# Kernel optimization log

Measured on AMD Instinct MI355X. Metric: run time of the kernel, lower is better.

Reference implementation:

```python
import jax, jax.numpy as jnp
import numpy as np

N, E, G, L, D = 50000, 800000, 512, 3, 128
BN_EPS = 1e-5


def setup_inputs() -> dict:
    key = jax.random.key(0)
    ks = jax.random.split(key, 16)
    x = jax.random.normal(ks[0], (N, D), dtype=jnp.float32)
    edge_index = jax.random.randint(ks[1], (2, E), 0, N)
    batch = jnp.sort(jax.random.randint(ks[2], (N,), 0, G))
    W1 = jax.random.normal(ks[3], (L, D, D), dtype=jnp.float32) * 0.05
    b1 = jax.random.normal(ks[4], (L, D), dtype=jnp.float32) * 0.05
    gamma = jax.random.uniform(ks[5], (L, D), dtype=jnp.float32) + 0.5
    beta = jax.random.normal(ks[6], (L, D), dtype=jnp.float32) * 0.05
    running_mean = jax.random.normal(ks[7], (L, D), dtype=jnp.float32) * 0.1
    running_var = jax.random.uniform(ks[8], (L, D), dtype=jnp.float32) + 0.5
    W2 = jax.random.normal(ks[9], (L, D, D), dtype=jnp.float32) * 0.05
    b2 = jax.random.normal(ks[10], (L, D), dtype=jnp.float32) * 0.05
    lin1_W = jax.random.normal(ks[11], (L * D, L * D), dtype=jnp.float32) * 0.05
    lin1_b = jax.random.normal(ks[12], (L * D,), dtype=jnp.float32) * 0.05
    lin2_W = jax.random.normal(ks[13], (L * D, 10), dtype=jnp.float32) * 0.05
    lin2_b = jax.random.normal(ks[14], (10,), dtype=jnp.float32) * 0.05
    return {"x": x, "edge_index": edge_index, "batch": batch,
            "W1": W1, "b1": b1, "gamma": gamma, "beta": beta,
            "running_mean": running_mean, "running_var": running_var,
            "W2": W2, "b2": b2, "lin1_W": lin1_W, "lin1_b": lin1_b,
            "lin2_W": lin2_W, "lin2_b": lin2_b}


def _gin_layer(h, src, dst, W1, b1, gamma, beta, rm, rv, W2, b2):
    # GINConv (eps=0): MLP((1+eps)*x + sum_{j->i} x_j); aggregate src->dst
    agg = jax.ops.segment_sum(h[src], dst, num_segments=N)  # [N, D]
    z = (h + agg) @ W1 + b1
    # BatchNorm1d in eval mode (running stats)
    z = (z - rm) * (gamma / jnp.sqrt(rv + BN_EPS)) + beta
    z = jax.nn.relu(z)
    return jax.nn.relu(z @ W2 + b2)


def reference(x, edge_index, batch, W1, b1, gamma, beta, running_mean,
              running_var, W2, b2, lin1_W, lin1_b, lin2_W, lin2_b):
    src, dst = edge_index[0], edge_index[1]
    h = x
    pooled = []
    for i in range(L):
        h = _gin_layer(h, src, dst, W1[i], b1[i], gamma[i], beta[i],
                       running_mean[i], running_var[i], W2[i], b2[i])
        pooled.append(jax.ops.segment_sum(h, batch, num_segments=G))  # [G, D]
    g = jnp.concatenate(pooled, axis=1)  # [G, L*D]
    g = jax.nn.relu(g @ lin1_W + lin1_b)
    # dropout is identity in eval mode
    return g @ lin2_W + lin2_b  # [G, num_classes]
```

## Files before the change

### kernel.cpp

```cpp
#include <hip/hip_runtime.h>
#include <hip/hip_bf16.h>

#define D_FEAT 128
#define N_GRAPHS 512
#define N_LAYERS 3
#define POOL_DIM (N_LAYERS * D_FEAT)
#define N_CLASSES 10
#define BN_EPS 1e-5f
#define CAP 64
#define NBINS 8
#define SLABCAP 768


typedef __attribute__((ext_vector_type(8))) short bf16x8;
typedef __attribute__((ext_vector_type(8))) unsigned short ushort8;
typedef __attribute__((ext_vector_type(4))) float f32x4;

__device__ __forceinline__ unsigned short f2bf(float f) {
    unsigned u = __builtin_bit_cast(unsigned, f);
    u += 0x7FFFu + ((u >> 16) & 1u);
    return (unsigned short)(u >> 16);
}
__device__ __forceinline__ float bf2f(unsigned short h) {
    unsigned u = ((unsigned)h) << 16;
    return __builtin_bit_cast(float, u);
}
__device__ __forceinline__ float bf_lo(unsigned u) {
    return __builtin_bit_cast(float, u << 16);
}
__device__ __forceinline__ float bf_hi(unsigned u) {
    return __builtin_bit_cast(float, u & 0xffff0000u);
}

__global__ __launch_bounds__(256) void setup_kernel(
        const float* __restrict__ x, unsigned short* __restrict__ xb,
        const float* __restrict__ W1, const float* __restrict__ W2,
        unsigned short* __restrict__ Wt,
        const float* __restrict__ b1, const float* __restrict__ gamma,
        const float* __restrict__ beta, const float* __restrict__ rm,
        const float* __restrict__ rv, const float* __restrict__ b2,
        float* __restrict__ ea, float* __restrict__ eb,
        int* __restrict__ cursor, float* __restrict__ pooled,
        const int* __restrict__ ei, int2* __restrict__ pairs,
        int* __restrict__ cnts, int E,
        int N, int n4, int B0, int B1, int B2, int B3, int B4) {
    int b = blockIdx.x, tid = threadIdx.x;
    if (b < B0) {
        int i = b * 256 + tid;
        if (i < n4) {
            float4 v = ((const float4*)x)[i];
            ushort4 o;
            o.x = f2bf(v.x); o.y = f2bf(v.y); o.z = f2bf(v.z); o.w = f2bf(v.w);
            ((ushort4*)xb)[i] = o;
        }
    } else if (b < B1) {
        __shared__ float tile[64][65];
        int t = b - B0;
        int slot = t >> 2;
        int r0 = ((t >> 1) & 1) * 64;
        int c0 = (t & 1) * 64;
        int l = slot >> 1;
        const float* W = (slot & 1) ? W2 : W1;
        const float* Wb = W + (size_t)l * D_FEAT * D_FEAT;
        int rr = tid >> 2, cc4 = (tid & 3) * 16;
        #pragma unroll
        for (int j = 0; j < 16; ++j)
            tile[rr][cc4 + j] = Wb[(size_t)(r0 + rr) * D_FEAT + c0 + cc4 + j];
        __syncthreads();
        int nn = tid >> 2, kk4 = (tid & 3) * 16;
        unsigned short* Wo = Wt + (size_t)slot * D_FEAT * D_FEAT;
        #pragma unroll
        for (int j = 0; j < 16; ++j)
            Wo[(size_t)(c0 + nn) * D_FEAT + r0 + kk4 + j] = f2bf(tile[kk4 + j][nn]);
    } else if (b < B2) {
        int i = (b - B1) * 256 + tid;
        if (i < N_LAYERS * D_FEAT) {
            int l = i >> 7, c = i & 127;
            float s = gamma[i] * rsqrtf(rv[i] + BN_EPS);
            ea[(2 * l) * D_FEAT + c] = s;
            eb[(2 * l) * D_FEAT + c] = (b1[i] - rm[i]) * s + beta[i];
            ea[(2 * l + 1) * D_FEAT + c] = 1.0f;
            eb[(2 * l + 1) * D_FEAT + c] = b2[i];
        }
    } else if (b < B3) {
        int i = (b - B2) * 256 + tid;
        if (i < N) cursor[i] = 0;
    } else if (b < B4) {
        int i = (b - B3) * 256 + tid;
        if (i < N_GRAPHS * POOL_DIM) pooled[i] = 0.f;
    } else {
        __shared__ int loc[NBINS];
        int bb = b - B4;
        int per = (E + 255) / 256;
        int e0 = bb * per;
        int e1 = e0 + per; if (e1 > E) e1 = E;
        int span = (N + NBINS - 1) / NBINS;
        if (tid < NBINS) loc[tid] = 0;
        __syncthreads();
        for (int e = e0 + tid; e < e1; e += 256) {
            int dst = ei[E + e];
            int src = ei[e];
            int bin = dst / span;
            int p = atomicAdd(&loc[bin], 1);
            if (p < SLABCAP)
                pairs[((size_t)(bin * 256 + bb)) * SLABCAP + p] = make_int2(src, dst);
        }
        __syncthreads();
        if (tid < NBINS)
            cnts[tid * 256 + bb] = loc[tid];
    }
}

__global__ __launch_bounds__(256) void fill_v3(const int2* __restrict__ pairs,
                                               const int* __restrict__ cnts,
                                               int* __restrict__ cursor,
                                               int* __restrict__ bucket) {
    int r = blockIdx.x & 7;
    int chunk = blockIdx.x >> 3;
    #pragma unroll
    for (int s = 0; s < 4; ++s) {
        int blk = chunk * 4 + s;
        int cnt = cnts[r * 256 + blk];
        if (cnt > SLABCAP) cnt = SLABCAP;
        const int2* slab = pairs + (size_t)(r * 256 + blk) * SLABCAP;
        for (int p = threadIdx.x; p < cnt; p += 256) {
            int2 pr = slab[p];
            int pos = atomicAdd(&cursor[pr.y], 1);
            if (pos < CAP) bucket[(size_t)pr.y * CAP + pos] = pr.x;
        }
    }
}

__global__ __launch_bounds__(256) void agg_kernel(const unsigned short* __restrict__ hprev,
                                                  const int* __restrict__ deg,
                                                  const int* __restrict__ bucket,
                                                  unsigned short* __restrict__ y, int n) {
    int wave = threadIdx.x >> 6, lane = threadIdx.x & 63;
    int n0 = (blockIdx.x * 4 + wave) * 2;
    if (n0 >= n) return;
    int n1 = n0 + 1;
    bool v1 = (n1 < n);
    int d0 = deg[n0]; if (d0 > CAP) d0 = CAP;
    int d1 = v1 ? deg[n1] : 0; if (d1 > CAP) d1 = CAP;
    int grp = lane >> 4, sub = lane & 15;
    const uint4* hp = (const uint4*)hprev;

    int idx0 = bucket[(size_t)n0 * CAP + lane];
    int idx1 = v1 ? bucket[(size_t)n1 * CAP + lane] : 0;

    uint4 s0v = hp[(size_t)n0 * 16 + sub];
    uint4 s1v = v1 ? hp[(size_t)n1 * 16 + sub] : make_uint4(0u, 0u, 0u, 0u);

    float a0[8] = {0.f,0.f,0.f,0.f,0.f,0.f,0.f,0.f};
    float a1[8] = {0.f,0.f,0.f,0.f,0.f,0.f,0.f,0.f};
    int dmax = d0 > d1 ? d0 : d1;

    auto issue = [&](int t, bool (&p0)[4], bool (&p1)[4],
                     uint4 (&w0)[4], uint4 (&w1)[4]) {
        #pragma unroll
        for (int q = 0; q < 4; ++q) {
            int e = t + q * 4 + grp;
            int s0 = __shfl(idx0, e & 63);
            int s1 = __shfl(idx1, e & 63);
            p0[q] = e < d0;
            p1[q] = e < d1;
            int r0 = p0[q] ? s0 : n0;
            int r1 = p1[q] ? s1 : n0;
            w0[q] = hp[(size_t)r0 * 16 + sub];
            w1[q] = hp[(size_t)r1 * 16 + sub];
        }
    };
    auto accum = [&](bool (&p0)[4], bool (&p1)[4],
                     uint4 (&w0)[4], uint4 (&w1)[4]) {
        #pragma unroll
        for (int q = 0; q < 4; ++q) {
            if (p0[q]) {
                uint4 v = w0[q];
                a0[0] += bf_lo(v.x); a0[1] += bf_hi(v.x);
                a0[2] += bf_lo(v.y); a0[3] += bf_hi(v.y);
                a0[4] += bf_lo(v.z); a0[5] += bf_hi(v.z);
                a0[6] += bf_lo(v.w); a0[7] += bf_hi(v.w);
            }
            if (p1[q]) {
                uint4 v = w1[q];
                a1[0] += bf_lo(v.x); a1[1] += bf_hi(v.x);
                a1[2] += bf_lo(v.y); a1[3] += bf_hi(v.y);
                a1[4] += bf_lo(v.z); a1[5] += bf_hi(v.z);
                a1[6] += bf_lo(v.w); a1[7] += bf_hi(v.w);
            }
        }
    };

    if (dmax > 0) {
        bool cp0[4], cp1[4];
        uint4 cw0[4], cw1[4];
        issue(0, cp0, cp1, cw0, cw1);
        for (int t = 16; t < dmax; t += 16) {
            bool np0[4], np1[4];
            uint4 nw0[4], nw1[4];
            issue(t, np0, np1, nw0, nw1);
            accum(cp0, cp1, cw0, cw1);
            #pragma unroll
            for (int q = 0; q < 4; ++q) {
                cp0[q] = np0[q]; cp1[q] = np1[q];
                cw0[q] = nw0[q]; cw1[q] = nw1[q];
            }
        }
        accum(cp0, cp1, cw0, cw1);
    }

    #pragma unroll
    for (int j = 0; j < 8; ++j) {
        a0[j] += __shfl_xor(a0[j], 16);
        a0[j] += __shfl_xor(a0[j], 32);
        a1[j] += __shfl_xor(a1[j], 16);
        a1[j] += __shfl_xor(a1[j], 32);
    }

    a0[0] += bf_lo(s0v.x); a0[1] += bf_hi(s0v.x);
    a0[2] += bf_lo(s0v.y); a0[3] += bf_hi(s0v.y);
    a0[4] += bf_lo(s0v.z); a0[5] += bf_hi(s0v.z);
    a0[6] += bf_lo(s0v.w); a0[7] += bf_hi(s0v.w);
    if (v1) {
        a1[0] += bf_lo(s1v.x); a1[1] += bf_hi(s1v.x);
        a1[2] += bf_lo(s1v.y); a1[3] += bf_hi(s1v.y);
        a1[4] += bf_lo(s1v.z); a1[5] += bf_hi(s1v.z);
        a1[6] += bf_lo(s1v.w); a1[7] += bf_hi(s1v.w);
    }

    if (grp == 0) {
        uint4 o;
        o.x = (unsigned)f2bf(a0[0]) | ((unsigned)f2bf(a0[1]) << 16);
        o.y = (unsigned)f2bf(a0[2]) | ((unsigned)f2bf(a0[3]) << 16);
        o.z = (unsigned)f2bf(a0[4]) | ((unsigned)f2bf(a0[5]) << 16);
        o.w = (unsigned)f2bf(a0[6]) | ((unsigned)f2bf(a0[7]) << 16);
        ((uint4*)y)[(size_t)n0 * 16 + sub] = o;
        if (v1) {
            uint4 p;
            p.x = (unsigned)f2bf(a1[0]) | ((unsigned)f2bf(a1[1]) << 16);
            p.y = (unsigned)f2bf(a1[2]) | ((unsigned)f2bf(a1[3]) << 16);
            p.z = (unsigned)f2bf(a1[4]) | ((unsigned)f2bf(a1[5]) << 16);
            p.w = (unsigned)f2bf(a1[6]) | ((unsigned)f2bf(a1[7]) << 16);
            ((uint4*)y)[(size_t)n1 * 16 + sub] = p;
        }
    }
}

__global__ __launch_bounds__(256) void layer_fused(const unsigned short* __restrict__ A,
                                                   const unsigned short* __restrict__ Wt1,
                                                   const unsigned short* __restrict__ Wt2,
                                                   const float* __restrict__ ea1,
                                                   const float* __restrict__ eb1,
                                                   const float* __restrict__ ea2,
                                                   const float* __restrict__ eb2,
                                                   const int* __restrict__ batch,
                                                   float* __restrict__ pooled, int loff,
                                                   unsigned short* __restrict__ outh, int n) {
    __shared__ unsigned short As[64][136];
    __shared__ unsigned short Ws[128][136];
    int tid = threadIdx.x;
    int row0 = blockIdx.x * 64;
    int wave = tid >> 6, lane = tid & 63;
    int m0 = wave * 16;
    int lrow = lane & 15, lq = lane >> 4;

    #pragma unroll
    for (int i = 0; i < 4; ++i) {
        int idx = tid + i * 256;
        int r = idx >> 4, c = (idx & 15) * 8;
        ushort8 v = (ushort8)0;
        if (row0 + r < n) v = *(const ushort8*)&A[(size_t)(row0 + r) * D_FEAT + c];
        *(ushort8*)&As[r][c] = v;
    }
    #pragma unroll
    for (int i = 0; i < 8; ++i) {
        int idx = tid + i * 256;
        int r = idx >> 4, c = (idx & 15) * 8;
        *(ushort8*)&Ws[r][c] = *(const ushort8*)&Wt1[(size_t)r * D_FEAT + c];
    }

    ushort8 w2reg[8];
    #pragma unroll
    for (int i = 0; i < 8; ++i) {
        int idx = tid + i * 256;
        int r = idx >> 4, c = (idx & 15) * 8;
        w2reg[i] = *(const ushort8*)&Wt2[(size_t)r * D_FEAT + c];
    }

    int gr0 = row0 + m0 + lq * 4;
    int bq[4];
    if (gr0 + 3 < n) {
        int4 b4 = *(const int4*)&batch[gr0];
        bq[0] = b4.x; bq[1] = b4.y; bq[2] = b4.z; bq[3] = b4.w;
    } else {
        #pragma unroll
        for (int r = 0; r < 4; ++r)
            bq[r] = (gr0 + r < n) ? batch[gr0 + r] : -1;
    }
    __syncthreads();

    f32x4 acc[8] = {};
    #pragma unroll
    for (int t = 0; t < 4; ++t) {
        bf16x8 a = *(const bf16x8*)&As[m0 + lrow][t * 32 + lq * 8];
        #pragma unroll
        for (int nt = 0; nt < 8; ++nt) {
            bf16x8 b = *(const bf16x8*)&Ws[nt * 16 + lrow][t * 32 + lq * 8];
            acc[nt] = __builtin_amdgcn_mfma_f32_16x16x32_bf16(a, b, acc[nt], 0, 0, 0);
        }
    }
    __syncthreads();

    #pragma unroll
    for (int nt = 0; nt < 8; ++nt) {
        int col = nt * 16 + lrow;
        float al = ea1[col], be = eb1[col];
        #pragma unroll
        for (int r = 0; r < 4; ++r) {
            float v = fmaxf(fmaf(acc[nt][r], al, be), 0.f);
            As[m0 + lq * 4 + r][col] = f2bf(v);
        }
    }
    #pragma unroll
    for (int i = 0; i < 8; ++i) {
        int idx = tid + i * 256;
        int r = idx >> 4, c = (idx & 15) * 8;
        *(ushort8*)&Ws[r][c] = w2reg[i];
    }
    __syncthreads();

    f32x4 acc2[8] = {};
    #pragma unroll
    for (int t = 0; t < 4; ++t) {
        bf16x8 a = *(const bf16x8*)&As[m0 + lrow][t * 32 + lq * 8];
        #pragma unroll
        for (int nt = 0; nt < 8; ++nt) {
            bf16x8 b = *(const bf16x8*)&Ws[nt * 16 + lrow][t * 32 + lq * 8];
            acc2[nt] = __builtin_amdgcn_mfma_f32_16x16x32_bf16(a, b, acc2[nt], 0, 0, 0);
        }
    }

    float vv[8][4];
    #pragma unroll
    for (int nt = 0; nt < 8; ++nt) {
        int col = nt * 16 + lrow;
        float al = ea2[col], be = eb2[col];
        #pragma unroll
        for (int r = 0; r < 4; ++r) {
            unsigned short hb = f2bf(fmaxf(fmaf(acc2[nt][r], al, be), 0.f));
            vv[nt][r] = bf2f(hb);
            if (outh) {
                int grow = row0 + m0 + lq * 4 + r;
                if (grow < n) outh[(size_t)grow * D_FEAT + col] = hb;
            }
        }
    }

    int gmn = 0x7fffffff, gmx = -1;
    #pragma unroll
    for (int r = 0; r < 4; ++r) {
        if (bq[r] >= 0) {
            gmn = bq[r] < gmn ? bq[r] : gmn;
            gmx = bq[r] > gmx ? bq[r] : gmx;
        }
    }
    {
        int t;
        t = __shfl_xor(gmn, 16); gmn = t < gmn ? t : gmn;
        t = __shfl_xor(gmn, 32); gmn = t < gmn ? t : gmn;
        t = __shfl_xor(gmx, 16); gmx = t > gmx ? t : gmx;
        t = __shfl_xor(gmx, 32); gmx = t > gmx ? t : gmx;
    }
    for (int seg = gmn; seg <= gmx; ++seg) {
        #pragma unroll
        for (int nt = 0; nt < 8; ++nt) {
            float s = 0.f;
            #pragma unroll
            for (int r = 0; r < 4; ++r)
                if (bq[r] == seg) s += vv[nt][r];
            s += __shfl_xor(s, 16);
            s += __shfl_xor(s, 32);
            if (lq == 0 && s != 0.f)
                atomicAdd(&pooled[(size_t)seg * POOL_DIM + loff + nt * 16 + lrow], s);
        }
    }
}

__global__ __launch_bounds__(384) void head_kernel(const float* __restrict__ pooled,
                                                   const float* __restrict__ W1,
                                                   const float* __restrict__ b1v,
                                                   const float* __restrict__ W2,
                                                   const float* __restrict__ b2v,
                                                   float* __restrict__ out) {
    __shared__ float f1[4][POOL_DIM];
    int j = threadIdx.x;
    int g0 = blockIdx.x * 4;
    const float* pr = pooled + (size_t)g0 * POOL_DIM;
    float bb = b1v[j];
    float s0 = bb, s1 = bb, s2 = bb, s3 = bb;
    for (int k0 = 0; k0 < POOL_DIM; k0 += 8) {
        float w[8];
        #pragma unroll
        for (int i = 0; i < 8; ++i)
            w[i] = W1[(size_t)(k0 + i) * POOL_DIM + j];
        #pragma unroll
        for (int i = 0; i < 8; ++i) {
            int k = k0 + i;
            s0 = fmaf(pr[k],                w[i], s0);
            s1 = fmaf(pr[POOL_DIM + k],     w[i], s1);
            s2 = fmaf(pr[2 * POOL_DIM + k], w[i], s2);
            s3 = fmaf(pr[3 * POOL_DIM + k], w[i], s3);
        }
    }
    f1[0][j] = fmaxf(s0, 0.f);
    f1[1][j] = fmaxf(s1, 0.f);
    f1[2][j] = fmaxf(s2, 0.f);
    f1[3][j] = fmaxf(s3, 0.f);
    __syncthreads();
    if (j < 4 * N_CLASSES) {
        int g = j / N_CLASSES, c = j % N_CLASSES;
        float s = b2v[c];
        for (int k = 0; k < POOL_DIM; ++k)
            s = fmaf(f1[g][k], W2[(size_t)k * N_CLASSES + c], s);
        out[(size_t)(g0 + g) * N_CLASSES + c] = s;
    }
}

extern "C" void kernel_launch(void* const* d_in, const int* in_sizes, int n_in,
                              void* d_out, int out_size, void* d_ws, size_t ws_size,
                              hipStream_t stream) {
    const float* x      = (const float*)d_in[0];
    const int*   ei     = (const int*)  d_in[1];
    const int*   batch  = (const int*)  d_in[2];
    const float* W1     = (const float*)d_in[3];
    const float* b1     = (const float*)d_in[4];
    const float* gamma  = (const float*)d_in[5];
    const float* beta   = (const float*)d_in[6];
    const float* rm     = (const float*)d_in[7];
    const float* rv     = (const float*)d_in[8];
    const float* W2     = (const float*)d_in[9];
    const float* b2     = (const float*)d_in[10];
    const float* lin1W  = (const float*)d_in[11];
    const float* lin1b  = (const float*)d_in[12];
    const float* lin2W  = (const float*)d_in[13];
    const float* lin2b  = (const float*)d_in[14];
    float* out = (float*)d_out;

    const int N = in_sizes[0] / D_FEAT;
    const int E = in_sizes[1] / 2;

    char* ws = (char*)d_ws;
    auto carve = [&](size_t bytes) {
        char* p = ws;
        ws += (bytes + 255) & ~(size_t)255;
        return p;
    };
    int*   cursor    = (int*)  carve((size_t)N * 4);
    int*   cnts      = (int*)  carve((size_t)NBINS * 256 * 4);
    int*   bucket    = (int*)  carve((size_t)N * CAP * 4);
    int2*  pairs     = (int2*) carve((size_t)NBINS * 256 * SLABCAP * 8);
    float* ea        = (float*)carve((size_t)2 * N_LAYERS * D_FEAT * 4);
    float* eb        = (float*)carve((size_t)2 * N_LAYERS * D_FEAT * 4);
    unsigned short* Wt   = (unsigned short*)carve((size_t)2 * N_LAYERS * D_FEAT * D_FEAT * 2);
    unsigned short* xb   = (unsigned short*)carve((size_t)N * D_FEAT * 2);
    unsigned short* ybuf = (unsigned short*)carve((size_t)N * D_FEAT * 2);
    unsigned short* hbuf = (unsigned short*)carve((size_t)N * D_FEAT * 2);
    float* pooled    = (float*)carve((size_t)N_GRAPHS * POOL_DIM * 4);

    const int n4 = N * D_FEAT / 4;
    const int B0 = (n4 + 255) / 256;
    const int B1 = B0 + 24;
    const int B2 = B1 + 2;
    const int B3 = B2 + (N + 255) / 256;
    const int B4 = B3 + (N_GRAPHS * POOL_DIM + 255) / 256;
    const int B5 = B4 + 256;

    setup_kernel<<<B5, 256, 0, stream>>>(x, xb, W1, W2, Wt, b1, gamma, beta,
                                         rm, rv, b2, ea, eb, cursor, pooled,
                                         ei, pairs, cnts, E,
                                         N, n4, B0, B1, B2, B3, B4);
    fill_v3<<<8 * 64, 256, 0, stream>>>(pairs, cnts, cursor, bucket);

    const unsigned short* hprev = xb;
    for (int l = 0; l < N_LAYERS; ++l) {
        agg_kernel<<<(N + 7) / 8, 256, 0, stream>>>(hprev, cursor, bucket, ybuf, N);
        unsigned short* outh = (l == N_LAYERS - 1) ? nullptr : hbuf;
        layer_fused<<<(N + 63) / 64, 256, 0, stream>>>(ybuf,
                      Wt + (size_t)(2 * l) * D_FEAT * D_FEAT,
                      Wt + (size_t)(2 * l + 1) * D_FEAT * D_FEAT,
                      ea + (size_t)(2 * l) * D_FEAT,
                      eb + (size_t)(2 * l) * D_FEAT,
                      ea + (size_t)(2 * l + 1) * D_FEAT,
                      eb + (size_t)(2 * l + 1) * D_FEAT,
                      batch, pooled, l * D_FEAT, outh, N);
        hprev = hbuf;
    }
    head_kernel<<<N_GRAPHS / 4, 384, 0, stream>>>(pooled, lin1W, lin1b, lin2W, lin2b, out);
}
```

Measured before the change: 329.2 us.

## Slice features into XCD-mapped column slabs for L2-resident neighbor gathers

Stores node features as four 32-column slabs (slice-major, node-major within each slice). The aggregation kernel maps each slice to a pair of XCDs by block index, so each XCD's L2 only has to hold one slab's gather working set. Neighbor indices shrink to 16-bit, which only works while N stays below 65536. The new kernel has 4 lanes per node with a software-prefetched 4-edge loop; the layer kernel's loads and stores are remapped to the sliced layout. This relies on round-robin block-to-XCD dispatch and makes the dense-kernel accesses less contiguous.

```diff
diff --git a/kernel.cpp b/kernel.cpp
--- a/kernel.cpp
+++ b/kernel.cpp
@@ -10,6 +10,7 @@
 #define CAP 64
 #define NBINS 8
 #define SLABCAP 768
+#define NSLICE 4
 
 
 typedef __attribute__((ext_vector_type(8))) short bf16x8;
@@ -51,7 +52,11 @@
             float4 v = ((const float4*)x)[i];
             ushort4 o;
             o.x = f2bf(v.x); o.y = f2bf(v.y); o.z = f2bf(v.z); o.w = f2bf(v.w);
-            ((ushort4*)xb)[i] = o;
+            int node = i >> 5;
+            int c4 = i & 31;
+            int sl = c4 >> 3;
+            int off = c4 & 7;
+            ((ushort4*)xb)[((size_t)sl * N + node) * 8 + off] = o;
         }
     } else if (b < B1) {
         __shared__ float tile[64][65];
@@ -114,7 +119,7 @@
 __global__ __launch_bounds__(256) void fill_v3(const int2* __restrict__ pairs,
                                                const int* __restrict__ cnts,
                                                int* __restrict__ cursor,
-                                               int* __restrict__ bucket) {
+                                               unsigned short* __restrict__ bucket) {
     int r = blockIdx.x & 7;
     int chunk = blockIdx.x >> 3;
     #pragma unroll
@@ -126,123 +131,91 @@
         for (int p = threadIdx.x; p < cnt; p += 256) {
             int2 pr = slab[p];
             int pos = atomicAdd(&cursor[pr.y], 1);
-            if (pos < CAP) bucket[(size_t)pr.y * CAP + pos] = pr.x;
-        }
-    }
-}
-
-__global__ __launch_bounds__(256) void agg_kernel(const unsigned short* __restrict__ hprev,
-                                                  const int* __restrict__ deg,
-                                                  const int* __restrict__ bucket,
-                                                  unsigned short* __restrict__ y, int n) {
+            if (pos < CAP)
+                bucket[(size_t)pr.y * CAP + pos] = (unsigned short)pr.x;
+        }
+    }
+}
+
+__global__ __launch_bounds__(256) void agg_slice(
+        const unsigned short* __restrict__ hs,
+        const int* __restrict__ deg,
+        const unsigned short* __restrict__ bucket,
+        unsigned short* __restrict__ ys,
+        int n, int nchunks) {
+    int xcd = blockIdx.x & 7;
+    int s = xcd >> 1;
+    int chunk = (blockIdx.x >> 3) * 2 + (xcd & 1);
+    if (chunk >= nchunks) return;
     int wave = threadIdx.x >> 6, lane = threadIdx.x & 63;
-    int n0 = (blockIdx.x * 4 + wave) * 2;
-    if (n0 >= n) return;
-    int n1 = n0 + 1;
-    bool v1 = (n1 < n);
-    int d0 = deg[n0]; if (d0 > CAP) d0 = CAP;
-    int d1 = v1 ? deg[n1] : 0; if (d1 > CAP) d1 = CAP;
-    int grp = lane >> 4, sub = lane & 15;
-    const uint4* hp = (const uint4*)hprev;
-
-    int idx0 = bucket[(size_t)n0 * CAP + lane];
-    int idx1 = v1 ? bucket[(size_t)n1 * CAP + lane] : 0;
-
-    uint4 s0v = hp[(size_t)n0 * 16 + sub];
-    uint4 s1v = v1 ? hp[(size_t)n1 * 16 + sub] : make_uint4(0u, 0u, 0u, 0u);
-
-    float a0[8] = {0.f,0.f,0.f,0.f,0.f,0.f,0.f,0.f};
-    float a1[8] = {0.f,0.f,0.f,0.f,0.f,0.f,0.f,0.f};
-    int dmax = d0 > d1 ? d0 : d1;
-
-    auto issue = [&](int t, bool (&p0)[4], bool (&p1)[4],
-                     uint4 (&w0)[4], uint4 (&w1)[4]) {
-        #pragma unroll
-        for (int q = 0; q < 4; ++q) {
-            int e = t + q * 4 + grp;
-            int s0 = __shfl(idx0, e & 63);
-            int s1 = __shfl(idx1, e & 63);
-            p0[q] = e < d0;
-            p1[q] = e < d1;
-            int r0 = p0[q] ? s0 : n0;
-            int r1 = p1[q] ? s1 : n0;
-            w0[q] = hp[(size_t)r0 * 16 + sub];
-            w1[q] = hp[(size_t)r1 * 16 + sub];
-        }
-    };
-    auto accum = [&](bool (&p0)[4], bool (&p1)[4],
-                     uint4 (&w0)[4], uint4 (&w1)[4]) {
-        #pragma unroll
-        for (int q = 0; q < 4; ++q) {
-            if (p0[q]) {
-                uint4 v = w0[q];
-                a0[0] += bf_lo(v.x); a0[1] += bf_hi(v.x);
-                a0[2] += bf_lo(v.y); a0[3] += bf_hi(v.y);
-                a0[4] += bf_lo(v.z); a0[5] += bf_hi(v.z);
-                a0[6] += bf_lo(v.w); a0[7] += bf_hi(v.w);
+    int grp = lane >> 2, sub = lane & 3;
+    int n0 = chunk * 64 + wave * 16 + grp;
+    bool valid = n0 < n;
+    int node = valid ? n0 : 0;
+    int d = valid ? deg[node] : 0;
+    if (d > CAP) d = CAP;
+
+    const uint4* h4 = (const uint4*)hs;
+    size_t sbase = (size_t)s * n * 4;
+    const unsigned short* brow = bucket + (size_t)node * CAP;
+
+    int dmax = d;
+    dmax = max(dmax, __shfl_xor(dmax, 4));
+    dmax = max(dmax, __shfl_xor(dmax, 8));
+    dmax = max(dmax, __shfl_xor(dmax, 16));
+    dmax = max(dmax, __shfl_xor(dmax, 32));
+
+    uint4 sv = h4[sbase + (size_t)node * 4 + sub];
+
+    float acc[8] = {0.f,0.f,0.f,0.f,0.f,0.f,0.f,0.f};
+
+    if (dmax > 0) {
+        int sA[4];
+        #pragma unroll
+        for (int u = 0; u < 4; ++u) {
+            sA[u] = node;
+            if (u < d) sA[u] = (int)brow[u];
+        }
+        for (int t = 0; t < dmax; t += 4) {
+            uint4 w[4];
+            #pragma unroll
+            for (int u = 0; u < 4; ++u) {
+                w[u] = make_uint4(0u, 0u, 0u, 0u);
+                if (t + u < d)
+                    w[u] = h4[sbase + (size_t)sA[u] * 4 + sub];
             }
-            if (p1[q]) {
-                uint4 v = w1[q];
-                a1[0] += bf_lo(v.x); a1[1] += bf_hi(v.x);
-                a1[2] += bf_lo(v.y); a1[3] += bf_hi(v.y);
-                a1[4] += bf_lo(v.z); a1[5] += bf_hi(v.z);
-                a1[6] += bf_lo(v.w); a1[7] += bf_hi(v.w);
+            int sB[4];
+            #pragma unroll
+            for (int u = 0; u < 4; ++u) {
+                int e = t + 4 + u;
+                sB[u] = node;
+                if (e < d) sB[u] = (int)brow[e];
             }
-        }
-    };
-
-    if (dmax > 0) {
-        bool cp0[4], cp1[4];
-        uint4 cw0[4], cw1[4];
-        issue(0, cp0, cp1, cw0, cw1);
-        for (int t = 16; t < dmax; t += 16) {
-            bool np0[4], np1[4];
-            uint4 nw0[4], nw1[4];
-            issue(t, np0, np1, nw0, nw1);
-            accum(cp0, cp1, cw0, cw1);
             #pragma unroll
-            for (int q = 0; q < 4; ++q) {
-                cp0[q] = np0[q]; cp1[q] = np1[q];
-                cw0[q] = nw0[q]; cw1[q] = nw1[q];
+            for (int u = 0; u < 4; ++u) {
+                uint4 v = w[u];
+                acc[0] += bf_lo(v.x); acc[1] += bf_hi(v.x);
+                acc[2] += bf_lo(v.y); acc[3] += bf_hi(v.y);
+                acc[4] += bf_lo(v.z); acc[5] += bf_hi(v.z);
+                acc[6] += bf_lo(v.w); acc[7] += bf_hi(v.w);
             }
-        }
-        accum(cp0, cp1, cw0, cw1);
-    }
-
-    #pragma unroll
-    for (int j = 0; j < 8; ++j) {
-        a0[j] += __shfl_xor(a0[j], 16);
-        a0[j] += __shfl_xor(a0[j], 32);
-        a1[j] += __shfl_xor(a1[j], 16);
-        a1[j] += __shfl_xor(a1[j], 32);
-    }
-
-    a0[0] += bf_lo(s0v.x); a0[1] += bf_hi(s0v.x);
-    a0[2] += bf_lo(s0v.y); a0[3] += bf_hi(s0v.y);
-    a0[4] += bf_lo(s0v.z); a0[5] += bf_hi(s0v.z);
-    a0[6] += bf_lo(s0v.w); a0[7] += bf_hi(s0v.w);
-    if (v1) {
-        a1[0] += bf_lo(s1v.x); a1[1] += bf_hi(s1v.x);
-        a1[2] += bf_lo(s1v.y); a1[3] += bf_hi(s1v.y);
-        a1[4] += bf_lo(s1v.z); a1[5] += bf_hi(s1v.z);
-        a1[6] += bf_lo(s1v.w); a1[7] += bf_hi(s1v.w);
-    }
-
-    if (grp == 0) {
+            #pragma unroll
+            for (int u = 0; u < 4; ++u) sA[u] = sB[u];
+        }
+    }
+
+    acc[0] += bf_lo(sv.x); acc[1] += bf_hi(sv.x);
+    acc[2] += bf_lo(sv.y); acc[3] += bf_hi(sv.y);
+    acc[4] += bf_lo(sv.z); acc[5] += bf_hi(sv.z);
+    acc[6] += bf_lo(sv.w); acc[7] += bf_hi(sv.w);
+
+    if (valid) {
         uint4 o;
-        o.x = (unsigned)f2bf(a0[0]) | ((unsigned)f2bf(a0[1]) << 16);
-        o.y = (unsigned)f2bf(a0[2]) | ((unsigned)f2bf(a0[3]) << 16);
-        o.z = (unsigned)f2bf(a0[4]) | ((unsigned)f2bf(a0[5]) << 16);
-        o.w = (unsigned)f2bf(a0[6]) | ((unsigned)f2bf(a0[7]) << 16);
-        ((uint4*)y)[(size_t)n0 * 16 + sub] = o;
-        if (v1) {
-            uint4 p;
-            p.x = (unsigned)f2bf(a1[0]) | ((unsigned)f2bf(a1[1]) << 16);
-            p.y = (unsigned)f2bf(a1[2]) | ((unsigned)f2bf(a1[3]) << 16);
-            p.z = (unsigned)f2bf(a1[4]) | ((unsigned)f2bf(a1[5]) << 16);
-            p.w = (unsigned)f2bf(a1[6]) | ((unsigned)f2bf(a1[7]) << 16);
-            ((uint4*)y)[(size_t)n1 * 16 + sub] = p;
-        }
+        o.x = (unsigned)f2bf(acc[0]) | ((unsigned)f2bf(acc[1]) << 16);
+        o.y = (unsigned)f2bf(acc[2]) | ((unsigned)f2bf(acc[3]) << 16);
+        o.z = (unsigned)f2bf(acc[4]) | ((unsigned)f2bf(acc[5]) << 16);
+        o.w = (unsigned)f2bf(acc[6]) | ((unsigned)f2bf(acc[7]) << 16);
+        ((uint4*)ys)[sbase + (size_t)node * 4 + sub] = o;
     }
 }
 
@@ -268,8 +241,10 @@
     for (int i = 0; i < 4; ++i) {
         int idx = tid + i * 256;
         int r = idx >> 4, c = (idx & 15) * 8;
+        int sl = c >> 5, off = c & 31;
         ushort8 v = (ushort8)0;
-        if (row0 + r < n) v = *(const ushort8*)&A[(size_t)(row0 + r) * D_FEAT + c];
+        if (row0 + r < n)
+            v = *(const ushort8*)&A[((size_t)sl * n + (row0 + r)) * 32 + off];
         *(ushort8*)&As[r][c] = v;
     }
     #pragma unroll
@@ -345,13 +320,15 @@
     for (int nt = 0; nt < 8; ++nt) {
         int col = nt * 16 + lrow;
         float al = ea2[col], be = eb2[col];
+        int sl = col >> 5, off = col & 31;
         #pragma unroll
         for (int r = 0; r < 4; ++r) {
             unsigned short hb = f2bf(fmaxf(fmaf(acc2[nt][r], al, be), 0.f));
             vv[nt][r] = bf2f(hb);
             if (outh) {
                 int grow = row0 + m0 + lq * 4 + r;
-                if (grow < n) outh[(size_t)grow * D_FEAT + col] = hb;
+                if (grow < n)
+                    outh[((size_t)sl * n + grow) * 32 + off] = hb;
             }
         }
     }
@@ -457,7 +434,7 @@
     };
     int*   cursor    = (int*)  carve((size_t)N * 4);
     int*   cnts      = (int*)  carve((size_t)NBINS * 256 * 4);
-    int*   bucket    = (int*)  carve((size_t)N * CAP * 4);
+    unsigned short* bucket = (unsigned short*)carve((size_t)N * CAP * 2);
     int2*  pairs     = (int2*) carve((size_t)NBINS * 256 * SLABCAP * 8);
     float* ea        = (float*)carve((size_t)2 * N_LAYERS * D_FEAT * 4);
     float* eb        = (float*)carve((size_t)2 * N_LAYERS * D_FEAT * 4);
@@ -481,9 +458,13 @@
                                          N, n4, B0, B1, B2, B3, B4);
     fill_v3<<<8 * 64, 256, 0, stream>>>(pairs, cnts, cursor, bucket);
 
+    const int nchunks = (N + 63) / 64;
+    const int gblocks = 8 * ((nchunks + 1) / 2);
+
     const unsigned short* hprev = xb;
     for (int l = 0; l < N_LAYERS; ++l) {
-        agg_kernel<<<(N + 7) / 8, 256, 0, stream>>>(hprev, cursor, bucket, ybuf, N);
+        agg_slice<<<gblocks, 256, 0, stream>>>(hprev, cursor, bucket, ybuf,
+                                               N, nchunks);
         unsigned short* outh = (l == N_LAYERS - 1) ? nullptr : hbuf;
         layer_fused<<<(N + 63) / 64, 256, 0, stream>>>(ybuf,
                       Wt + (size_t)(2 * l) * D_FEAT * D_FEAT,
```

New measurement: 349.6 us. +6.2%, slower.
